# Optimization experiments

Measured on AMD Instinct MI355X. Metric: run time of the kernel, lower is better.

Reference implementation:

```python
import jax, jax.numpy as jnp
import numpy as np

EPS = 1e-09
TOP_K = 2


def setup_inputs() -> dict:
    key = jax.random.key(0)
    k1, k2 = jax.random.split(key)
    N, D, E = 32768, 1024, 64
    x = jax.random.normal(k1, (N, D), dtype=jnp.float32)
    gate_w = jax.random.normal(k2, (E, D), dtype=jnp.float32) * (1.0 / np.sqrt(D))
    return {"x": x, "gate_w": gate_w}


def reference(x, gate_w):
    # logits: [N, E] = x @ gate_w.T  (nn.Linear with no bias)
    logits = jnp.einsum("nd,ed->ne", x, gate_w)
    probs = jax.nn.softmax(logits, axis=-1)
    # aux load-balancing loss (stored on buffer in torch; returned here)
    mean_probs = probs.mean(axis=0)  # [E]
    aux_loss = jnp.sum(mean_probs * jnp.log(mean_probs + EPS))
    # top-k selection + renormalize
    top_k_weights, top_k_indices = jax.lax.top_k(probs, TOP_K)  # [N, K]
    top_k_weights = top_k_weights / (top_k_weights.sum(axis=-1, keepdims=True) + EPS)
    return top_k_weights, top_k_indices, aux_loss
```

## Files before the change

kernel.cpp:

```cpp
#include <hip/hip_runtime.h>
#include <math.h>

#define NROWS 32768
#define DDIM  1024
#define NEXP  64
#define TAU   2e-4f
#define EPSF  1e-9f
#define CAPMAX 8192
#define NSHARD 8

typedef __attribute__((ext_vector_type(8)))  short  short8;
typedef __attribute__((ext_vector_type(16))) float  f32x16;
typedef __attribute__((address_space(3))) unsigned int       lds_u32;
typedef __attribute__((address_space(1))) const unsigned int g_u32;

__device__ __forceinline__ bool gt_(float a, int ea, float b, int eb)
{ return a > b || (a == b && ea < eb); }

__device__ __forceinline__ void cvt_hl(float f, unsigned short& h, unsigned short& l)
{
    unsigned u  = __float_as_uint(f);
    unsigned hu = (u + 0x7FFFu + ((u >> 16) & 1u)) & 0xFFFF0000u;
    h = (unsigned short)(hu >> 16);
    float r = f - __uint_as_float(hu);
    unsigned v = __float_as_uint(r);
    l = (unsigned short)((v + 0x7FFFu + ((v >> 16) & 1u)) >> 16);
}

__global__ void wpack_kernel(const float* __restrict__ gw,
                             unsigned short* __restrict__ wp,
                             float* __restrict__ shard,
                             int* __restrict__ cnt)
{
    if (blockIdx.x == 0) {
        shard[threadIdx.x]       = 0.0f;
        shard[256 + threadIdx.x] = 0.0f;
        if (threadIdx.x == 0) *cnt = 0;
    }
    const int kc = blockIdx.x;
    const int t  = threadIdx.x;
    const int lane = t & 63, g = (t >> 6) & 1, pr = t >> 7;
    const int e = g * 32 + (lane & 31);
    const int k = kc * 16 + (lane >> 5) * 8;
    float4 f0 = *reinterpret_cast<const float4*>(gw + (size_t)e * DDIM + k);
    float4 f1 = *reinterpret_cast<const float4*>(gw + (size_t)e * DDIM + k + 4);
    float f[8] = {f0.x, f0.y, f0.z, f0.w, f1.x, f1.y, f1.z, f1.w};
    short8 o;
    #pragma unroll
    for (int j = 0; j < 8; ++j) {
        unsigned short hh, ll;
        cvt_hl(f[j], hh, ll);
        o[j] = pr ? (short)ll : (short)hh;
    }
    *reinterpret_cast<short8*>(wp + ((size_t)((kc * 2 + g) * 2 + pr) * 64 + lane) * 8) = o;
}

__global__ __launch_bounds__(256, 2) void moe_main(
    const float* __restrict__ x, const unsigned short* __restrict__ wp,
    float* __restrict__ out, float* __restrict__ shard,
    int* __restrict__ cnt, int* __restrict__ list, int cap)
{
    extern __shared__ char smem[];

    const int t = threadIdx.x;
    const int wave = t >> 6, lane = t & 63;
    const int wm = wave & 1, g = wave >> 1;
    const int l31 = lane & 31, l5 = lane >> 5;
    const int row0 = blockIdx.x * 64;
    const int arow = wm * 32 + l31;

    f32x16 acc;
    #pragma unroll
    for (int r = 0; r < 16; ++r) acc[r] = 0.0f;

    #define STAGE(xb, bb, c_) do {                                               \
        const char* xs0_ = (const char*)x + (size_t)row0 * 4096 + (size_t)(c_) * 256; \
        const char* bs0_ = (const char*)wp + (size_t)(c_) * 16384;               \
        _Pragma("unroll")                                                        \
        for (int q_ = 0; q_ < 4; ++q_) {                                         \
            int d_ = q_ * 4096 + t * 16;                                         \
            int sw_ = d_ ^ (((d_ >> 8) & 7) << 5);                               \
            const char* xsrc_ = xs0_ + (size_t)(sw_ >> 8) * 4096 + (sw_ & 255);  \
            __builtin_amdgcn_global_load_lds((g_u32*)xsrc_,                      \
                (lds_u32*)(smem + (xb) + d_), 16, 0, 0);                         \
            __builtin_amdgcn_global_load_lds((g_u32*)(bs0_ + d_),                \
                (lds_u32*)(smem + (bb) + d_), 16, 0, 0);                         \
        }                                                                        \
    } while (0)

    STAGE(0, 32768, 0);

    for (int c = 0; c < 16; ++c) {
        const int xb = (c & 1) * 16384;
        const int bb = 32768 + (c & 1) * 16384;
        if (c < 15) {
            STAGE(((c + 1) & 1) * 16384, 32768 + ((c + 1) & 1) * 16384, c + 1);
            __builtin_amdgcn_sched_barrier(0);
            asm volatile("s_waitcnt vmcnt(8)" ::: "memory");
        } else {
            asm volatile("s_waitcnt vmcnt(0)" ::: "memory");
        }
        __builtin_amdgcn_s_barrier();
        __builtin_amdgcn_sched_barrier(0);

        #pragma unroll
        for (int j = 0; j < 4; ++j) {
            int lb = arow * 256 + j * 64 + l5 * 32;
            lb ^= ((arow & 7) << 5);
            const float* ap = reinterpret_cast<const float*>(smem + xb + lb);
            float4 f0 = *reinterpret_cast<const float4*>(ap);
            float4 f1 = *reinterpret_cast<const float4*>(ap + 4);
            float f[8] = {f0.x, f0.y, f0.z, f0.w, f1.x, f1.y, f1.z, f1.w};
            short8 ah, al;
            #pragma unroll
            for (int jj = 0; jj < 8; ++jj) {
                unsigned short hh, ll;
                cvt_hl(f[jj], hh, ll);
                ah[jj] = (short)hh; al[jj] = (short)ll;
            }
            const char* bp = smem + bb + ((j * 2 + g) * 2) * 1024 + lane * 16;
            short8 bh = *reinterpret_cast<const short8*>(bp);
            short8 bl = *reinterpret_cast<const short8*>(bp + 1024);
            acc = __builtin_amdgcn_mfma_f32_32x32x16_bf16(ah, bh, acc, 0, 0, 0);
            acc = __builtin_amdgcn_mfma_f32_32x32x16_bf16(al, bh, acc, 0, 0, 0);
            acc = __builtin_amdgcn_mfma_f32_32x32x16_bf16(ah, bl, acc, 0, 0, 0);
        }
        __builtin_amdgcn_sched_barrier(0);
        __builtin_amdgcn_s_barrier();
        __builtin_amdgcn_sched_barrier(0);
    }
    #undef STAGE

    float* lgs = reinterpret_cast<float*>(smem);
    __syncthreads();
    #pragma unroll
    for (int r = 0; r < 16; ++r) {
        const int lrow = wm * 32 + (r & 3) + 8 * (r >> 2) + 4 * l5;
        lgs[lrow * 68 + g * 32 + l31] = acc[r];
    }
    __syncthreads();

    const int erow = t >> 2, q = t & 3;
    float L[16];
    #pragma unroll
    for (int i = 0; i < 4; ++i) {
        float4 v = *reinterpret_cast<const float4*>(lgs + erow * 68 + q * 16 + i * 4);
        L[4*i] = v.x; L[4*i+1] = v.y; L[4*i+2] = v.z; L[4*i+3] = v.w;
    }
    float v1 = -3.4e38f, v2 = -3.4e38f, v3 = -3.4e38f;
    int   e1 = 1 << 30,  e2 = 1 << 30,  e3 = 1 << 30;
    #pragma unroll
    for (int i = 0; i < 16; ++i) {
        float v = L[i]; int e = q * 16 + i;
        if      (gt_(v, e, v1, e1)) { v3=v2; e3=e2; v2=v1; e2=e1; v1=v; e1=e; }
        else if (gt_(v, e, v2, e2)) { v3=v2; e3=e2; v2=v; e2=e; }
        else if (gt_(v, e, v3, e3)) { v3=v; e3=e; }
    }
    #pragma unroll
    for (int m = 1; m <= 2; m <<= 1) {
        float o1 = __shfl_xor(v1, m), o2 = __shfl_xor(v2, m), o3 = __shfl_xor(v3, m);
        int  oe1 = __shfl_xor(e1, m), oe2 = __shfl_xor(e2, m), oe3 = __shfl_xor(e3, m);
        float n1, n2, n3; int m1, m2, m3;
        if (gt_(v1, e1, o1, oe1)) {
            n1 = v1; m1 = e1;
            if (gt_(v2, e2, o1, oe1)) {
                n2 = v2; m2 = e2;
                if (gt_(v3, e3, o1, oe1)) { n3 = v3; m3 = e3; } else { n3 = o1; m3 = oe1; }
            } else {
                n2 = o1; m2 = oe1;
                if (gt_(v2, e2, o2, oe2)) { n3 = v2; m3 = e2; } else { n3 = o2; m3 = oe2; }
            }
        } else {
            n1 = o1; m1 = oe1;
            if (gt_(o2, oe2, v1, e1)) {
                n2 = o2; m2 = oe2;
                if (gt_(o3, oe3, v1, e1)) { n3 = o3; m3 = oe3; } else { n3 = v1; m3 = e1; }
            } else {
                n2 = v1; m2 = e1;
                if (gt_(o2, oe2, v2, e2)) { n3 = o2; m3 = oe2; } else { n3 = v2; m3 = e2; }
            }
        }
        v1 = n1; e1 = m1; v2 = n2; e2 = m2; v3 = n3; e3 = m3;
    }
    float pr[16], sl = 0.0f;
    #pragma unroll
    for (int i = 0; i < 16; ++i) { pr[i] = expf(L[i] - v1); sl += pr[i]; }
    float S = sl;
    S += __shfl_xor(S, 1); S += __shfl_xor(S, 2);
    const float invS = 1.0f / S;
    #pragma unroll
    for (int i = 0; i < 16; ++i) pr[i] *= invS;
    #pragma unroll
    for (int m = 4; m <= 32; m <<= 1)
        #pragma unroll
        for (int i = 0; i < 16; ++i) pr[i] += __shfl_xor(pr[i], m);
    float* auxred = lgs + 64 * 68;
    if (lane < 4) {
        #pragma unroll
        for (int i = 0; i < 16; ++i) auxred[wave * 64 + q * 16 + i] = pr[i];
    }
    if (q == 0) {
        const float p1 = invS;
        const float p2 = expf(v2 - v1) * invS;
        const float dn = p1 + p2 + EPSF;
        const int r = row0 + erow;
        out[2 * r]                 = p1 / dn;
        out[2 * r + 1]             = p2 / dn;
        out[2 * NROWS + 2 * r]     = (float)e1;
        out[2 * NROWS + 2 * r + 1] = (float)e2;
        if (cap > 0 && (v1 - v2 < TAU || v2 - v3 < TAU)) {
            int pos = atomicAdd(cnt, 1);
            if (pos < cap) list[pos] = r;
        }
    }
    __syncthreads();
    if (t < 64) {
        float s = auxred[t] + auxred[64 + t] + auxred[128 + t] + auxred[192 + t];
        atomicAdd(&shard[(blockIdx.x & (NSHARD - 1)) * 64 + t], s);
    }
}

__global__ __launch_bounds__(256) void finalize_kernel(
    const float* __restrict__ x, const float* __restrict__ gw,
    float* __restrict__ out, const float* __restrict__ shard,
    const int* __restrict__ cnt, const int* __restrict__ list, int cap)
{
    if (blockIdx.x == 0) {
        const int tt = threadIdx.x;
        if (tt < 64) {
            float m = 0.0f;
            #pragma unroll
            for (int s = 0; s < NSHARD; ++s) m += shard[s * 64 + tt];
            m *= (1.0f / (float)NROWS);
            float v = m * logf(m + EPSF);
            #pragma unroll
            for (int k = 1; k <= 32; k <<= 1) v += __shfl_xor(v, k);
            if (tt == 0) out[4 * NROWS] = v;
        }
        return;
    }
    __shared__ float lg[64];
    const int n = (cap > 0) ? min(*cnt, cap) : 0;
    const int tt = threadIdx.x, e = tt >> 2, part = tt & 3;
    for (int j = (int)blockIdx.x - 1; j < n; j += 64) {
        const int row = list[j];
        const float* xr = x  + (size_t)row * DDIM + part * 256;
        const float* wr = gw + (size_t)e   * DDIM + part * 256;
        float a = 0.0f;
        #pragma unroll 8
        for (int kk = 0; kk < 64; ++kk) {
            float4 xv = *reinterpret_cast<const float4*>(xr + kk * 4);
            float4 wv = *reinterpret_cast<const float4*>(wr + kk * 4);
            a += xv.x * wv.x + xv.y * wv.y + xv.z * wv.z + xv.w * wv.w;
        }
        a += __shfl_xor(a, 1); a += __shfl_xor(a, 2);
        if (part == 0) lg[e] = a;
        __syncthreads();
        if (tt < 4) {
            const int q = tt;
            float v1 = -3.4e38f, v2 = -3.4e38f; int e1 = 1 << 30, e2 = 1 << 30;
            float Lr[16];
            #pragma unroll
            for (int i = 0; i < 16; ++i) {
                float v = Lr[i] = lg[q * 16 + i]; int ee = q * 16 + i;
                if      (gt_(v, ee, v1, e1)) { v2 = v1; e2 = e1; v1 = v; e1 = ee; }
                else if (gt_(v, ee, v2, e2)) { v2 = v; e2 = ee; }
            }
            #pragma unroll
            for (int m = 1; m <= 2; m <<= 1) {
                float o1 = __shfl_xor(v1, m), o2 = __shfl_xor(v2, m);
                int  oe1 = __shfl_xor(e1, m), oe2 = __shfl_xor(e2, m);
                float n1, n2; int m1, m2;
                if (gt_(v1, e1, o1, oe1)) {
                    n1 = v1; m1 = e1;
                    if (gt_(v2, e2, o1, oe1)) { n2 = v2; m2 = e2; } else { n2 = o1; m2 = oe1; }
                } else {
                    n1 = o1; m1 = oe1;
                    if (gt_(o2, oe2, v1, e1)) { n2 = o2; m2 = oe2; } else { n2 = v1; m2 = e1; }
                }
                v1 = n1; e1 = m1; v2 = n2; e2 = m2;
            }
            float s = 0.0f;
            #pragma unroll
            for (int i = 0; i < 16; ++i) s += expf(Lr[i] - v1);
            s += __shfl_xor(s, 1); s += __shfl_xor(s, 2);
            if (q == 0) {
                const float invS = 1.0f / s;
                const float p1 = invS, p2 = expf(v2 - v1) * invS;
                const float dn = p1 + p2 + EPSF;
                out[2 * row]                 = p1 / dn;
                out[2 * row + 1]             = p2 / dn;
                out[2 * NROWS + 2 * row]     = (float)e1;
                out[2 * NROWS + 2 * row + 1] = (float)e2;
            }
        }
        __syncthreads();
    }
}

extern "C" void kernel_launch(void* const* d_in, const int* in_sizes, int n_in,
                              void* d_out, int out_size, void* d_ws, size_t ws_size,
                              hipStream_t stream)
{
    const float* x  = (const float*)d_in[0];
    const float* gw = (const float*)d_in[1];
    float* out      = (float*)d_out;

    unsigned short* wp = (unsigned short*)d_ws;
    float* shard   = (float*)((char*)d_ws + 262144);
    int*   cnt     = (int*)((char*)d_ws + 264192);
    int*   list    = (int*)((char*)d_ws + 264448);
    int cap = 0;
    if (ws_size >= 264448 + 4096) {
        size_t avail = (ws_size - 264448) / sizeof(int);
        cap = (avail > CAPMAX) ? CAPMAX : (int)avail;
    }

    hipLaunchKernelGGL(wpack_kernel, dim3(64), dim3(256), 0, stream,
                       gw, wp, shard, cnt);
    hipLaunchKernelGGL(moe_main, dim3(NROWS / 64), dim3(256), 65536, stream,
                       x, wp, out, shard, cnt, list, cap);
    hipLaunchKernelGGL(finalize_kernel, dim3(65), dim3(256), 0, stream,
                       x, gw, out, shard, cnt, list, cap);
}
```

Baseline: 62.42 us.

## Deepen main-loop prefetch to four smaller stages and use hardware bf16 conversion

The GEMM main loop moves from a double buffer of 16 chunks (256 B of K each) to a four-slot ring of 32 chunks (128 B of K each). Three chunks are kept in flight, with vmcnt waits adjusted for the tail. The goal is to hide more global-load latency, at the cost of twice as many barriers per K and a new XOR swizzle on 128-byte rows. The hand-written bf16 hi/lo split is also replaced with __float2bfloat16, which may lower to a native conversion instruction and shorten the conversion ALU work per element.

```diff
diff --git a/kernel.cpp b/kernel.cpp
--- a/kernel.cpp
+++ b/kernel.cpp
@@ -1,4 +1,5 @@
 #include <hip/hip_runtime.h>
+#include <hip/hip_bf16.h>
 #include <math.h>
 
 #define NROWS 32768
@@ -8,6 +9,7 @@
 #define EPSF  1e-9f
 #define CAPMAX 8192
 #define NSHARD 8
+#define NCH   32
 
 typedef __attribute__((ext_vector_type(8)))  short  short8;
 typedef __attribute__((ext_vector_type(16))) float  f32x16;
@@ -17,14 +19,13 @@
 __device__ __forceinline__ bool gt_(float a, int ea, float b, int eb)
 { return a > b || (a == b && ea < eb); }
 
-__device__ __forceinline__ void cvt_hl(float f, unsigned short& h, unsigned short& l)
-{
-    unsigned u  = __float_as_uint(f);
-    unsigned hu = (u + 0x7FFFu + ((u >> 16) & 1u)) & 0xFFFF0000u;
-    h = (unsigned short)(hu >> 16);
-    float r = f - __uint_as_float(hu);
-    unsigned v = __float_as_uint(r);
-    l = (unsigned short)((v + 0x7FFFu + ((v >> 16) & 1u)) >> 16);
+__device__ __forceinline__ void cvt_hl(float f, short& h, short& l)
+{
+    __hip_bfloat16 hb = __float2bfloat16(f);
+    float r = f - __bfloat162float(hb);
+    __hip_bfloat16 lb = __float2bfloat16(r);
+    h = *reinterpret_cast<short*>(&hb);
+    l = *reinterpret_cast<short*>(&lb);
 }
 
 __global__ void wpack_kernel(const float* __restrict__ gw,
@@ -48,9 +49,9 @@
     short8 o;
     #pragma unroll
     for (int j = 0; j < 8; ++j) {
-        unsigned short hh, ll;
+        short hh, ll;
         cvt_hl(f[j], hh, ll);
-        o[j] = pr ? (short)ll : (short)hh;
+        o[j] = pr ? ll : hh;
     }
     *reinterpret_cast<short8*>(wp + ((size_t)((kc * 2 + g) * 2 + pr) * 64 + lane) * 8) = o;
 }
@@ -68,57 +69,70 @@
     const int l31 = lane & 31, l5 = lane >> 5;
     const int row0 = blockIdx.x * 64;
     const int arow = wm * 32 + l31;
+    const int xr   = (arow & 7) << 4;
 
     f32x16 acc;
     #pragma unroll
     for (int r = 0; r < 16; ++r) acc[r] = 0.0f;
 
-    #define STAGE(xb, bb, c_) do {                                               \
-        const char* xs0_ = (const char*)x + (size_t)row0 * 4096 + (size_t)(c_) * 256; \
-        const char* bs0_ = (const char*)wp + (size_t)(c_) * 16384;               \
+    int srow[2], scol[2];
+    #pragma unroll
+    for (int q = 0; q < 2; ++q) {
+        int d = q * 4096 + t * 16;
+        srow[q] = d >> 7;
+        scol[q] = (d & 127) ^ ((srow[q] & 7) << 4);
+    }
+
+    #define STAGE(c_) do {                                                       \
+        const char* xs0_ = (const char*)x + (size_t)row0 * 4096 + (size_t)(c_) * 128; \
+        const char* bs0_ = (const char*)wp + (size_t)(c_) * 8192;                \
+        const int xb_ = ((c_) & 3) * 8192;                                       \
+        const int bb_ = 32768 + ((c_) & 3) * 8192;                               \
         _Pragma("unroll")                                                        \
-        for (int q_ = 0; q_ < 4; ++q_) {                                         \
+        for (int q_ = 0; q_ < 2; ++q_) {                                         \
             int d_ = q_ * 4096 + t * 16;                                         \
-            int sw_ = d_ ^ (((d_ >> 8) & 7) << 5);                               \
-            const char* xsrc_ = xs0_ + (size_t)(sw_ >> 8) * 4096 + (sw_ & 255);  \
+            const char* xsrc_ = xs0_ + (size_t)srow[q_] * 4096 + scol[q_];       \
             __builtin_amdgcn_global_load_lds((g_u32*)xsrc_,                      \
-                (lds_u32*)(smem + (xb) + d_), 16, 0, 0);                         \
+                (lds_u32*)(smem + xb_ + d_), 16, 0, 0);                          \
             __builtin_amdgcn_global_load_lds((g_u32*)(bs0_ + d_),                \
-                (lds_u32*)(smem + (bb) + d_), 16, 0, 0);                         \
+                (lds_u32*)(smem + bb_ + d_), 16, 0, 0);                          \
         }                                                                        \
     } while (0)
 
-    STAGE(0, 32768, 0);
-
-    for (int c = 0; c < 16; ++c) {
-        const int xb = (c & 1) * 16384;
-        const int bb = 32768 + (c & 1) * 16384;
-        if (c < 15) {
-            STAGE(((c + 1) & 1) * 16384, 32768 + ((c + 1) & 1) * 16384, c + 1);
+    STAGE(0); STAGE(1); STAGE(2);
+
+    for (int i = 0; i < NCH; ++i) {
+        if (i < NCH - 3) {
+            STAGE(i + 3);
             __builtin_amdgcn_sched_barrier(0);
+            asm volatile("s_waitcnt vmcnt(12)" ::: "memory");
+        } else if (i == NCH - 3) {
             asm volatile("s_waitcnt vmcnt(8)" ::: "memory");
+        } else if (i == NCH - 2) {
+            asm volatile("s_waitcnt vmcnt(4)" ::: "memory");
         } else {
             asm volatile("s_waitcnt vmcnt(0)" ::: "memory");
         }
         __builtin_amdgcn_s_barrier();
         __builtin_amdgcn_sched_barrier(0);
 
+        const int xb = (i & 3) * 8192;
+        const int bb = 32768 + (i & 3) * 8192;
         #pragma unroll
-        for (int j = 0; j < 4; ++j) {
-            int lb = arow * 256 + j * 64 + l5 * 32;
-            lb ^= ((arow & 7) << 5);
-            const float* ap = reinterpret_cast<const float*>(smem + xb + lb);
-            float4 f0 = *reinterpret_cast<const float4*>(ap);
-            float4 f1 = *reinterpret_cast<const float4*>(ap + 4);
+        for (int kcl = 0; kcl < 2; ++kcl) {
+            const int cb = kcl * 64 + l5 * 32;
+            const char* xrow = smem + xb + arow * 128;
+            float4 f0 = *reinterpret_cast<const float4*>(xrow + (cb ^ xr));
+            float4 f1 = *reinterpret_cast<const float4*>(xrow + ((cb + 16) ^ xr));
             float f[8] = {f0.x, f0.y, f0.z, f0.w, f1.x, f1.y, f1.z, f1.w};
             short8 ah, al;
             #pragma unroll
             for (int jj = 0; jj < 8; ++jj) {
-                unsigned short hh, ll;
+                short hh, ll;
                 cvt_hl(f[jj], hh, ll);
-                ah[jj] = (short)hh; al[jj] = (short)ll;
-            }
-            const char* bp = smem + bb + ((j * 2 + g) * 2) * 1024 + lane * 16;
+                ah[jj] = hh; al[jj] = ll;
+            }
+            const char* bp = smem + bb + ((kcl * 2 + g) * 2) * 1024 + lane * 16;
             short8 bh = *reinterpret_cast<const short8*>(bp);
             short8 bl = *reinterpret_cast<const short8*>(bp + 1024);
             acc = __builtin_amdgcn_mfma_f32_32x32x16_bf16(ah, bh, acc, 0, 0, 0);
@@ -244,13 +258,13 @@
     const int tt = threadIdx.x, e = tt >> 2, part = tt & 3;
     for (int j = (int)blockIdx.x - 1; j < n; j += 64) {
         const int row = list[j];
-        const float* xr = x  + (size_t)row * DDIM + part * 256;
-        const float* wr = gw + (size_t)e   * DDIM + part * 256;
+        const float* xrp = x  + (size_t)row * DDIM + part * 256;
+        const float* wrp = gw + (size_t)e   * DDIM + part * 256;
         float a = 0.0f;
         #pragma unroll 8
         for (int kk = 0; kk < 64; ++kk) {
-            float4 xv = *reinterpret_cast<const float4*>(xr + kk * 4);
-            float4 wv = *reinterpret_cast<const float4*>(wr + kk * 4);
+            float4 xv = *reinterpret_cast<const float4*>(xrp + kk * 4);
+            float4 wv = *reinterpret_cast<const float4*>(wrp + kk * 4);
             a += xv.x * wv.x + xv.y * wv.y + xv.z * wv.z + xv.w * wv.w;
         }
         a += __shfl_xor(a, 1); a += __shfl_xor(a, 2);
```

After: 61.03 us. 2.2% less time.
